# Kernel optimization log

Hardware: AMD Instinct MI355X
Metric: run time of the kernel (lower is better)

Reference implementation:

```python
import jax, jax.numpy as jnp
import numpy as np

B, N, M, D, HEADS, L, DFF, TSTEPS = 8, 1024, 512, 128, 8, 6, 512, 100
S = N + M
HD = D // HEADS


def _layer_norm(x, g, b):
    mu = jnp.mean(x, axis=-1, keepdims=True)
    var = jnp.var(x, axis=-1, keepdims=True)
    return (x - mu) * jax.lax.rsqrt(var + 1e-5) * g + b


def setup_inputs() -> dict:
    rng = np.random.default_rng(0)
    # sparse parity-check matrix, ~6 ones per check row
    H = (rng.random((M, N)) < 6.0 / N).astype(np.float32)
    # create_mask with n_rings=1: eye(S) plus variable<->check Tanner edges
    conn = np.eye(S, dtype=np.float32)
    conn[N:, :N] = np.maximum(conn[N:, :N], H)
    conn[:N, N:] = np.maximum(conn[:N, N:], H.T)
    mask = ~(conn > 0)  # True = attention blocked (src_mask semantics)

    key = jax.random.key(0)
    ks = jax.random.split(key, 16)
    s = 0.05  # weight init scale ~ 1/sqrt(d_model)
    return {
        "r_t": jax.random.normal(ks[0], (B, N), jnp.float32),
        "t": jax.random.randint(ks[1], (B,), 0, TSTEPS),
        "pcm": jnp.asarray(H.astype(np.int32)),
        "mask": jnp.asarray(mask),
        "src_embed": jax.random.uniform(ks[2], (S, D), jnp.float32),
        "time_table": jax.random.normal(ks[3], (TSTEPS, D), jnp.float32),
        "Wq": jax.random.normal(ks[4], (L, D, D), jnp.float32) * s,
        "Wk": jax.random.normal(ks[5], (L, D, D), jnp.float32) * s,
        "Wv": jax.random.normal(ks[6], (L, D, D), jnp.float32) * s,
        "Wo": jax.random.normal(ks[7], (L, D, D), jnp.float32) * s,
        "W1": jax.random.normal(ks[8], (L, D, DFF), jnp.float32) * s,
        "W2": jax.random.normal(ks[9], (L, DFF, D), jnp.float32) * s,
        "g1": jnp.ones((L, D), jnp.float32),
        "b1": jnp.zeros((L, D), jnp.float32),
        "g2": jnp.ones((L, D), jnp.float32),
        "b2": jnp.zeros((L, D), jnp.float32),
        "fc_w": jax.random.normal(ks[10], (D, 1), jnp.float32) * s,
        "fc_b": jnp.zeros((1,), jnp.float32),
    }


def reference(r_t, t, pcm, mask, src_embed, time_table, Wq, Wk, Wv, Wo,
              W1, W2, g1, b1, g2, b2, fc_w, fc_b):
    # to_bin: BPSK sign -> bit {0,1}
    bits = 0.5 * (1.0 - jnp.sign(r_t))                       # [B, N]
    syn = (bits @ pcm.T.astype(jnp.float32)) % 2.0           # mod-2 syndrome [B, M]
    nodes = jnp.concatenate([jnp.abs(r_t), syn], axis=-1)    # [B, S]
    x = src_embed[None, :, :] * nodes[:, :, None]            # [B, S, D]
    te = time_table[t]                                       # [B, D] time embedding
    x = te[:, None, :] * x                                   # time-modulated input
    bias = jnp.where(mask, -1e9, 0.0)[None, None]            # [1, 1, S, S]
    inv_sqrt_hd = 1.0 / jnp.sqrt(jnp.float32(HD))
    for l in range(L):
        h = _layer_norm(x, g1[l], b1[l])
        q = (h @ Wq[l]).reshape(B, S, HEADS, HD)
        k = (h @ Wk[l]).reshape(B, S, HEADS, HD)
        v = (h @ Wv[l]).reshape(B, S, HEADS, HD)
        scores = jnp.einsum('bqhd,bkhd->bhqk', q, k) * inv_sqrt_hd + bias
        p = jax.nn.softmax(scores, axis=-1)
        o = jnp.einsum('bhqk,bkhd->bqhd', p, v).reshape(B, S, D)
        x = x + o @ Wo[l]
        # FiLM-style time conditioning on the FFN branch
        h2 = _layer_norm(x, g2[l], b2[l]) * te[:, None, :]
        x = x + jax.nn.relu(h2 @ W1[l]) @ W2[l]
    return x @ fc_w + fc_b                                   # z_hat [B, S, 1]
```

## Files before the change

### kernel.cpp

```cpp
#include <hip/hip_runtime.h>
#include <cmath>
#include <cstdint>

constexpr int B_ = 8, N_ = 1024, M_ = 512, D_ = 128, S_ = 1536, L_ = 6, DFF_ = 512;
constexpr int ROWS = B_ * S_;
constexpr int MAXDEG = 64;
constexpr int LKEY = 32;
constexpr int RPB  = 48;
constexpr int NBLK = ROWS / RPB;
constexpr int BPB  = S_ / RPB;
constexpr int NTILE = 12;
constexpr int TILE  = 128 * 128;
constexpr int KVSZ  = ROWS * 256;

typedef __bf16 bf16x8 __attribute__((ext_vector_type(8)));
typedef float  f32x4  __attribute__((ext_vector_type(4)));
typedef unsigned short u16x8 __attribute__((ext_vector_type(8)));

__device__ inline unsigned short f2bf(float f) {
  unsigned u = __float_as_uint(f);
  u += 0x7fffu + ((u >> 16) & 1u);
  return (unsigned short)(u >> 16);
}
__device__ inline float bf2f(unsigned short u) {
  return __uint_as_float(((unsigned)u) << 16);
}

__device__ __forceinline__ void async_ld16(const unsigned short* g, unsigned short* l) {
  __builtin_amdgcn_global_load_lds(
      (const __attribute__((address_space(1))) unsigned int*)(uintptr_t)g,
      (__attribute__((address_space(3))) unsigned int*)(unsigned)(uintptr_t)l,
      16, 0, 0);
}
__device__ __forceinline__ void issue_tile(const unsigned short* tp, unsigned short* bs,
                                           int w, int lane) {
  for (int c = w; c < 32; c += 6)
    async_ld16(tp + c * 512 + lane * 8, bs + c * 512);
}

__global__ void adj_init(int* __restrict__ adj, int* __restrict__ adjcnt) {
  int s = blockIdx.x * blockDim.x + threadIdx.x;
  if (s < S_) { adj[s * MAXDEG] = s; adjcnt[s] = 1; }
}
__global__ void adj_build(const int* __restrict__ pcm, int* __restrict__ adj,
                          int* __restrict__ adjcnt) {
  int c = blockIdx.x;
  int lane = threadIdx.x;
  const int* row = pcm + c * N_;
  for (int base = 0; base < N_; base += 64) {
    int k = base + lane;
    if (row[k] != 0) {
      int s1 = atomicAdd(&adjcnt[N_ + c], 1);
      if (s1 < MAXDEG) adj[(N_ + c) * MAXDEG + s1] = k;
      int s2 = atomicAdd(&adjcnt[k], 1);
      if (s2 < MAXDEG) adj[k * MAXDEG + s2] = N_ + c;
    }
  }
}

__global__ void xinit_kernel(const float* __restrict__ r_t, const int* __restrict__ adj,
                             const int* __restrict__ adjcnt, const float* __restrict__ se,
                             const int* __restrict__ tt, const float* __restrict__ table,
                             float* __restrict__ x, unsigned* __restrict__ barrier_cnt) {
  int bs = blockIdx.x;
  int b = bs / S_, s = bs % S_;
  int d = threadIdx.x;
  if (bs < 8 && d == 0)
    __hip_atomic_store(barrier_cnt + bs * 32, 0u, __ATOMIC_RELAXED, __HIP_MEMORY_SCOPE_AGENT);
  float node;
  if (s < N_) {
    node = fabsf(r_t[b * N_ + s]);
  } else {
    int cnt = adjcnt[s]; cnt = cnt < MAXDEG ? cnt : MAXDEG;
    float sum = 0.f;
    for (int j = 0; j < cnt; ++j) {
      int k = adj[s * MAXDEG + j];
      if (k < N_) {
        float r = r_t[b * N_ + k];
        sum += (r < 0.f) ? 1.f : (r > 0.f ? 0.f : 0.5f);
      }
    }
    node = fmodf(sum, 2.0f);
  }
  x[(size_t)bs * D_ + d] = table[tt[b] * D_ + d] * se[s * D_ + d] * node;
}

constexpr int WLAYER = NTILE * TILE;

__global__ void wconv_kernel(const float* __restrict__ Wq, const float* __restrict__ Wk,
                             const float* __restrict__ Wv, const float* __restrict__ Wo,
                             const float* __restrict__ W1, const float* __restrict__ W2,
                             unsigned short* __restrict__ out) {
  __shared__ unsigned short tl[128 * 130];
  int bid = blockIdx.x;
  int l = bid / NTILE, tile = bid % NTILE;
  const float* src;
  int rstride, coff = 0;
  if (tile == 0)      { src = Wk + (size_t)l * D_ * D_;  rstride = D_; }
  else if (tile == 1) { src = Wv + (size_t)l * D_ * D_;  rstride = D_; }
  else if (tile == 2) { src = Wq + (size_t)l * D_ * D_;  rstride = D_; }
  else if (tile == 3) { src = Wo + (size_t)l * D_ * D_;  rstride = D_; }
  else {
    int c = (tile - 4) >> 1;
    if (((tile - 4) & 1) == 0) { src = W1 + (size_t)l * D_ * DFF_; rstride = DFF_; coff = c * 128; }
    else                       { src = W2 + (size_t)l * DFF_ * D_ + (size_t)c * 128 * D_; rstride = D_; }
  }
  for (int i = threadIdx.x; i < 16384; i += 256) {
    int kd = i >> 7, rr = i & 127;
    tl[kd * 130 + rr] = f2bf(src[(size_t)kd * rstride + coff + rr]);
  }
  __syncthreads();
  unsigned short* o = out + (size_t)bid * TILE;
  for (int i = threadIdx.x; i < 16384; i += 256) {
    int rr = i >> 7;
    int sw = (i >> 3) & 15, e = i & 7;
    int kd = (sw ^ (rr & 15)) * 8 + e;
    o[i] = tl[kd * 130 + rr];
  }
}

__device__ __forceinline__ void mfma4(const unsigned short* As, const unsigned short* Bs,
                                      int rowbase, int colbase, int quad, int l16,
                                      f32x4 (&acc)[4]) {
#pragma unroll
  for (int kk = 0; kk < 4; ++kk) {
    int cb = kk * 4 + quad;
    int row = rowbase + l16;
    bf16x8 a = __builtin_bit_cast(bf16x8, *(const uint4*)&As[row * 128 + ((cb ^ (row & 15)) << 3)]);
    bf16x8 bb[4];
#pragma unroll
    for (int ct = 0; ct < 4; ++ct) {
      int n = colbase + ct * 16 + l16;
      bb[ct] = __builtin_bit_cast(bf16x8, *(const uint4*)&Bs[n * 128 + ((cb ^ (n & 15)) << 3)]);
    }
#pragma unroll
    for (int ct = 0; ct < 4; ++ct)
      acc[ct] = __builtin_amdgcn_mfma_f32_16x16x32_bf16(a, bb[ct], acc[ct], 0, 0, 0);
  }
}

__device__ __forceinline__ void grid_barrier(unsigned* cnt, unsigned target) {
  __syncthreads();
  if (threadIdx.x == 0) {
    __hip_atomic_fetch_add(cnt, 1u, __ATOMIC_RELAXED, __HIP_MEMORY_SCOPE_AGENT);
    while (__hip_atomic_load(cnt, __ATOMIC_RELAXED, __HIP_MEMORY_SCOPE_AGENT) < target)
      __builtin_amdgcn_s_sleep(4);
  }
  __syncthreads();
}

__global__ void __launch_bounds__(384) mega_kernel(
    const float* __restrict__ x0, unsigned short* __restrict__ kvbase,
    const unsigned short* __restrict__ wbf,
    const float* __restrict__ g1, const float* __restrict__ b1,
    const float* __restrict__ g2, const float* __restrict__ b2,
    const int* __restrict__ tt, const float* __restrict__ table,
    const int* __restrict__ adj, const int* __restrict__ adjc,
    const float* __restrict__ fcw, const float* __restrict__ fcb,
    float* __restrict__ out, unsigned* barrier_cnt) {
  __shared__ unsigned short As[RPB * 128];
  __shared__ unsigned short Bs[3][TILE];
  __shared__ unsigned short Cs[RPB * 128];
  __shared__ unsigned short KVs[RPB * 256];
  __shared__ float red1[2][RPB], red2[2][RPB];
  __shared__ int sKeys[RPB * LKEY];
  __shared__ int sCnt[RPB];
  const int row0 = blockIdx.x * RPB;
  const int b = row0 / S_;
  const int bS = b * S_;
  const int t = threadIdx.x, w = t >> 6, lane = t & 63, quad = lane >> 4, l16 = lane & 15;
  const int wr = w >> 1, wc = w & 1;
  const int rowbase = wr * 16, colbase = wc * 64;
  const int tbase = tt[b] * D_;
  unsigned* bcnt = barrier_cnt + b * 32;

  issue_tile(wbf + 0 * TILE, Bs[0], w, lane);
  issue_tile(wbf + 1 * TILE, Bs[1], w, lane);
  issue_tile(wbf + 2 * TILE, Bs[2], w, lane);

  f32x4 xreg[4];
#pragma unroll
  for (int ct = 0; ct < 4; ++ct)
#pragma unroll
    for (int i = 0; i < 4; ++i) {
      int row = row0 + rowbase + quad * 4 + i;
      int col = colbase + ct * 16 + l16;
      xreg[ct][i] = x0[(size_t)row * D_ + col];
    }
  if (t < RPB) {
    int c = adjc[row0 + t - bS];
    sCnt[t] = c < MAXDEG ? c : MAXDEG;
  }
  for (int i = t; i < RPB * LKEY; i += 384) {
    int r = i / LKEY, j = i % LKEY;
    sKeys[i] = adj[(row0 + r - bS) * MAXDEG + j];
  }

  for (int l = 0; l < L_; ++l) {
    const unsigned short* wt = wbf + (size_t)l * WLAYER;
    const float* g1l = g1 + l * D_;
    const float* b1l = b1 + l * D_;
    const float* g2l = g2 + l * D_;
    const float* b2l = b2 + l * D_;
    unsigned short* kv = kvbase + (size_t)l * KVSZ;

    float mu1[4], rs1[4];
#pragma unroll
    for (int i = 0; i < 4; ++i) {
      float s = 0.f, sq = 0.f;
#pragma unroll
      for (int ct = 0; ct < 4; ++ct) { s += xreg[ct][i]; sq += xreg[ct][i] * xreg[ct][i]; }
      for (int off = 1; off < 16; off <<= 1) { s += __shfl_xor(s, off); sq += __shfl_xor(sq, off); }
      if (l16 == 0) { red1[wc][rowbase + quad * 4 + i] = s; red2[wc][rowbase + quad * 4 + i] = sq; }
    }
    __syncthreads();
#pragma unroll
    for (int i = 0; i < 4; ++i) {
      int r = rowbase + quad * 4 + i;
      float mu = (red1[0][r] + red1[1][r]) * (1.f / 128.f);
      float var = (red2[0][r] + red2[1][r]) * (1.f / 128.f) - mu * mu;
      mu1[i] = mu;
      rs1[i] = rsqrtf(var + 1e-5f);
    }
#pragma unroll
    for (int ct = 0; ct < 4; ++ct)
#pragma unroll
      for (int i = 0; i < 4; ++i) {
        int rowL = rowbase + quad * 4 + i;
        int col = colbase + ct * 16 + l16;
        float h = (xreg[ct][i] - mu1[i]) * rs1[i] * g1l[col] + b1l[col];
        As[rowL * 128 + (((col >> 3) ^ (rowL & 15)) << 3) + (col & 7)] = f2bf(h);
      }
    __syncthreads();

    {
      f32x4 acc[4];
#pragma unroll
      for (int j = 0; j < 4; ++j) acc[j] = f32x4{0.f, 0.f, 0.f, 0.f};
      mfma4(As, Bs[0], rowbase, colbase, quad, l16, acc);
#pragma unroll
      for (int ct = 0; ct < 4; ++ct)
#pragma unroll
        for (int i = 0; i < 4; ++i) {
          int rowL = rowbase + quad * 4 + i;
          KVs[rowL * 256 + colbase + ct * 16 + l16] = f2bf(acc[ct][i]);
        }
    }
    {
      f32x4 acc[4];
#pragma unroll
      for (int j = 0; j < 4; ++j) acc[j] = f32x4{0.f, 0.f, 0.f, 0.f};
      mfma4(As, Bs[1], rowbase, colbase, quad, l16, acc);
#pragma unroll
      for (int ct = 0; ct < 4; ++ct)
#pragma unroll
        for (int i = 0; i < 4; ++i) {
          int rowL = rowbase + quad * 4 + i;
          KVs[rowL * 256 + 128 + colbase + ct * 16 + l16] = f2bf(acc[ct][i]);
        }
    }
    {
      f32x4 acc[4];
#pragma unroll
      for (int j = 0; j < 4; ++j) acc[j] = f32x4{0.f, 0.f, 0.f, 0.f};
      mfma4(As, Bs[2], rowbase, colbase, quad, l16, acc);
#pragma unroll
      for (int ct = 0; ct < 4; ++ct)
#pragma unroll
        for (int i = 0; i < 4; ++i) {
          int rowL = rowbase + quad * 4 + i;
          int col = colbase + ct * 16 + l16;
          Cs[rowL * 128 + (((col >> 3) ^ (rowL & 15)) << 3) + (col & 7)] = f2bf(acc[ct][i]);
        }
    }
    __syncthreads();
    for (int i = t; i < RPB * 128; i += 384) {
      int rL = i >> 7, cw = i & 127;
      unsigned u = *(const unsigned*)&KVs[rL * 256 + cw * 2];
      __hip_atomic_store((unsigned*)&kv[(size_t)(row0 + rL) * 256 + cw * 2],
                         u, __ATOMIC_RELAXED, __HIP_MEMORY_SCOPE_AGENT);
    }

    grid_barrier(bcnt, (unsigned)(BPB * (l + 1)));

    issue_tile(wt + 3 * TILE, Bs[0], w, lane);
    issue_tile(wt + 4 * TILE, Bs[1], w, lane);
    issue_tile(wt + 5 * TILE, Bs[2], w, lane);

    {
      const int rL = t >> 3, h = t & 7;
      const int s = row0 + rL - bS;
      const int cnt = sCnt[rL];
      float q[16];
      {
        u16x8 qa = *(const u16x8*)&Cs[rL * 128 + (((2 * h) ^ (rL & 15)) << 3)];
        u16x8 qb = *(const u16x8*)&Cs[rL * 128 + (((2 * h + 1) ^ (rL & 15)) << 3)];
#pragma unroll
        for (int j = 0; j < 8; ++j) { q[j] = bf2f(qa[j]); q[8 + j] = bf2f(qb[j]); }
      }
      float m = -1e30f, lsum = 0.f;
      float o16[16];
#pragma unroll
      for (int j = 0; j < 16; ++j) o16[j] = 0.f;
      for (int jb = 0; jb < cnt; jb += 4) {
        u16x8 K[4][2], V[4][2];
#pragma unroll
        for (int u = 0; u < 4; ++u) {
          int j = jb + u;
          int key = 0;
          if (j < cnt) key = (j < LKEY) ? sKeys[rL * LKEY + j] : adj[s * MAXDEG + j];
          const u16x8* kp = (const u16x8*)(kv + (size_t)(bS + key) * 256 + h * 16);
          K[u][0] = kp[0];  K[u][1] = kp[1];
          V[u][0] = kp[16]; V[u][1] = kp[17];
        }
#pragma unroll
        for (int u = 0; u < 4; ++u) {
          float dot = 0.f;
#pragma unroll
          for (int j = 0; j < 8; ++j) {
            dot = fmaf(q[j], bf2f(K[u][0][j]), dot);
            dot = fmaf(q[8 + j], bf2f(K[u][1][j]), dot);
          }
          dot *= 0.25f;
          if (jb + u >= cnt) dot = -1e30f;
          const float mn = fmaxf(m, dot);
          const float rescale = __expf(m - mn);
          const float e = __expf(dot - mn);
          lsum = lsum * rescale + e;
#pragma unroll
          for (int j = 0; j < 8; ++j) {
            o16[j]     = o16[j]     * rescale + e * bf2f(V[u][0][j]);
            o16[8 + j] = o16[8 + j] * rescale + e * bf2f(V[u][1][j]);
          }
          m = mn;
        }
      }
      const float inv = 1.f / lsum;
      u16x8 pk0, pk1;
#pragma unroll
      for (int j = 0; j < 8; ++j) {
        pk0[j] = f2bf(o16[j] * inv);
        pk1[j] = f2bf(o16[8 + j] * inv);
      }
      *(u16x8*)&As[rL * 128 + (((2 * h) ^ (rL & 15)) << 3)] = pk0;
      *(u16x8*)&As[rL * 128 + (((2 * h + 1) ^ (rL & 15)) << 3)] = pk1;
    }
    __syncthreads();

    f32x4 acc1[4];
#pragma unroll
    for (int j = 0; j < 4; ++j) acc1[j] = f32x4{0.f, 0.f, 0.f, 0.f};
    mfma4(As, Bs[0], rowbase, colbase, quad, l16, acc1);
    f32x4 xp[4];
#pragma unroll
    for (int ct = 0; ct < 4; ++ct)
#pragma unroll
      for (int i = 0; i < 4; ++i) xp[ct][i] = xreg[ct][i] + acc1[ct][i];
    float mu_[4], rs_[4];
#pragma unroll
    for (int i = 0; i < 4; ++i) {
      float s = 0.f, sq = 0.f;
#pragma unroll
      for (int ct = 0; ct < 4; ++ct) { s += xp[ct][i]; sq += xp[ct][i] * xp[ct][i]; }
      for (int off = 1; off < 16; off <<= 1) { s += __shfl_xor(s, off); sq += __shfl_xor(sq, off); }
      if (l16 == 0) { red1[wc][rowbase + quad * 4 + i] = s; red2[wc][rowbase + quad * 4 + i] = sq; }
    }
    __syncthreads();
#pragma unroll
    for (int i = 0; i < 4; ++i) {
      int r = rowbase + quad * 4 + i;
      float mu = (red1[0][r] + red1[1][r]) * (1.f / 128.f);
      float var = (red2[0][r] + red2[1][r]) * (1.f / 128.f) - mu * mu;
      mu_[i] = mu;
      rs_[i] = rsqrtf(var + 1e-5f);
    }
#pragma unroll
    for (int ct = 0; ct < 4; ++ct)
#pragma unroll
      for (int i = 0; i < 4; ++i) {
        int rowL = rowbase + quad * 4 + i;
        int col = colbase + ct * 16 + l16;
        float h2 = (xp[ct][i] - mu_[i]) * rs_[i] * g2l[col] + b2l[col];
        h2 *= table[tbase + col];
        As[rowL * 128 + (((col >> 3) ^ (rowL & 15)) << 3) + (col & 7)] = f2bf(h2);
      }
    __syncthreads();

    f32x4 acc2[4];
#pragma unroll
    for (int j = 0; j < 4; ++j) acc2[j] = f32x4{0.f, 0.f, 0.f, 0.f};
    const int bufW1[4] = {1, 0, 2, 1};
    const int bufW2[4] = {2, 1, 0, 2};
#pragma unroll
    for (int c = 0; c < 4; ++c) {
      f32x4 accF[4];
#pragma unroll
      for (int j = 0; j < 4; ++j) accF[j] = f32x4{0.f, 0.f, 0.f, 0.f};
      mfma4(As, Bs[bufW1[c]], rowbase, colbase, quad, l16, accF);
#pragma unroll
      for (int ct = 0; ct < 4; ++ct)
#pragma unroll
        for (int i = 0; i < 4; ++i) {
          int rowL = rowbase + quad * 4 + i;
          int col = colbase + ct * 16 + l16;
          Cs[rowL * 128 + (((col >> 3) ^ (rowL & 15)) << 3) + (col & 7)] =
              f2bf(fmaxf(accF[ct][i], 0.f));
        }
      __syncthreads();
      if (c < 3) issue_tile(wt + (4 + 2 * (c + 1)) * TILE, Bs[bufW1[c + 1]], w, lane);
      else if (l < L_ - 1) issue_tile(wt + WLAYER + 0 * TILE, Bs[0], w, lane);
      mfma4(Cs, Bs[bufW2[c]], rowbase, colbase, quad, l16, acc2);
      __syncthreads();
      if (c < 3) issue_tile(wt + (5 + 2 * (c + 1)) * TILE, Bs[bufW2[c + 1]], w, lane);
      else if (l < L_ - 1) {
        issue_tile(wt + WLAYER + 1 * TILE, Bs[1], w, lane);
        issue_tile(wt + WLAYER + 2 * TILE, Bs[2], w, lane);
      }
    }
    if (l < L_ - 1) {
#pragma unroll
      for (int ct = 0; ct < 4; ++ct)
#pragma unroll
        for (int i = 0; i < 4; ++i) xreg[ct][i] = xp[ct][i] + acc2[ct][i];
    } else {
      float pr[4] = {0.f, 0.f, 0.f, 0.f};
#pragma unroll
      for (int ct = 0; ct < 4; ++ct)
#pragma unroll
        for (int i = 0; i < 4; ++i)
          pr[i] += (xp[ct][i] + acc2[ct][i]) * fcw[colbase + ct * 16 + l16];
#pragma unroll
      for (int i = 0; i < 4; ++i) {
        float s = pr[i];
        for (int off = 1; off < 16; off <<= 1) s += __shfl_xor(s, off);
        if (l16 == 0) red1[wc][rowbase + quad * 4 + i] = s;
      }
      __syncthreads();
      if (wc == 0 && l16 == 0)
#pragma unroll
        for (int i = 0; i < 4; ++i) {
          int r = rowbase + quad * 4 + i;
          out[row0 + r] = red1[0][r] + red1[1][r] + fcb[0];
        }
    }
  }
}

extern "C" void kernel_launch(void* const* d_in, const int* in_sizes, int n_in,
                              void* d_out, int out_size, void* d_ws, size_t ws_size,
                              hipStream_t stream) {
  const float* r_t       = (const float*)d_in[0];
  const int*   t         = (const int*)d_in[1];
  const int*   pcm       = (const int*)d_in[2];
  const float* src_embed = (const float*)d_in[4];
  const float* time_tab  = (const float*)d_in[5];
  const float* Wq = (const float*)d_in[6];
  const float* Wk = (const float*)d_in[7];
  const float* Wv = (const float*)d_in[8];
  const float* Wo = (const float*)d_in[9];
  const float* W1 = (const float*)d_in[10];
  const float* W2 = (const float*)d_in[11];
  const float* g1 = (const float*)d_in[12];
  const float* b1 = (const float*)d_in[13];
  const float* g2 = (const float*)d_in[14];
  const float* b2 = (const float*)d_in[15];
  const float* fc_w = (const float*)d_in[16];
  const float* fc_b = (const float*)d_in[17];
  float* out = (float*)d_out;

  char* ws = (char*)d_ws;
  size_t off = 0;
  auto alloc = [&](size_t bytes) -> void* {
    void* p = ws + off;
    off = (off + bytes + 255) & ~(size_t)255;
    return p;
  };
  float*          x    = (float*)alloc((size_t)ROWS * D_ * 4);
  unsigned short* kv   = (unsigned short*)alloc((size_t)L_ * KVSZ * 2);
  int*            adj  = (int*)alloc((size_t)S_ * MAXDEG * 4);
  int*            adjc = (int*)alloc((size_t)S_ * 4);
  unsigned short* wbf  = (unsigned short*)alloc((size_t)L_ * WLAYER * 2);
  unsigned*       bcnt = (unsigned*)alloc(8 * 32 * 4);

  adj_init<<<(S_ + 255) / 256, 256, 0, stream>>>(adj, adjc);
  adj_build<<<M_, 64, 0, stream>>>(pcm, adj, adjc);
  wconv_kernel<<<L_ * NTILE, 256, 0, stream>>>(Wq, Wk, Wv, Wo, W1, W2, wbf);
  xinit_kernel<<<ROWS, 128, 0, stream>>>(r_t, adj, adjc, src_embed, t, time_tab, x, bcnt);

  mega_kernel<<<NBLK, 384, 0, stream>>>(x, kv, wbf, g1, b1, g2, b2,
                                        t, time_tab, adj, adjc, fc_w, fc_b, out, bcnt);
}
```

Baseline: 260.0 us.

## Fuse adjacency init into weight conversion and input embedding into mega kernel

Removes the adj_init and xinit kernels. Adjacency initialisation and the barrier-counter reset move into the first blocks of wconv_kernel. The syndrome and embedding computation of the initial x moves into mega_kernel's prologue using the staged adjacency keys. This cuts two kernel launches and the write and re-read of the full fp32 x buffer. In exchange, each mega_kernel block does a short serial per-row syndrome loop before its first layer.

Measured after the change: 255.3 us. About the same (-1.8%).

```diff
diff --git a/kernel.cpp b/kernel.cpp
--- a/kernel.cpp
+++ b/kernel.cpp
@@ -38,10 +38,6 @@
     async_ld16(tp + c * 512 + lane * 8, bs + c * 512);
 }
 
-__global__ void adj_init(int* __restrict__ adj, int* __restrict__ adjcnt) {
-  int s = blockIdx.x * blockDim.x + threadIdx.x;
-  if (s < S_) { adj[s * MAXDEG] = s; adjcnt[s] = 1; }
-}
 __global__ void adj_build(const int* __restrict__ pcm, int* __restrict__ adj,
                           int* __restrict__ adjcnt) {
   int c = blockIdx.x;
@@ -58,41 +54,22 @@
   }
 }
 
-__global__ void xinit_kernel(const float* __restrict__ r_t, const int* __restrict__ adj,
-                             const int* __restrict__ adjcnt, const float* __restrict__ se,
-                             const int* __restrict__ tt, const float* __restrict__ table,
-                             float* __restrict__ x, unsigned* __restrict__ barrier_cnt) {
-  int bs = blockIdx.x;
-  int b = bs / S_, s = bs % S_;
-  int d = threadIdx.x;
-  if (bs < 8 && d == 0)
-    __hip_atomic_store(barrier_cnt + bs * 32, 0u, __ATOMIC_RELAXED, __HIP_MEMORY_SCOPE_AGENT);
-  float node;
-  if (s < N_) {
-    node = fabsf(r_t[b * N_ + s]);
-  } else {
-    int cnt = adjcnt[s]; cnt = cnt < MAXDEG ? cnt : MAXDEG;
-    float sum = 0.f;
-    for (int j = 0; j < cnt; ++j) {
-      int k = adj[s * MAXDEG + j];
-      if (k < N_) {
-        float r = r_t[b * N_ + k];
-        sum += (r < 0.f) ? 1.f : (r > 0.f ? 0.f : 0.5f);
-      }
-    }
-    node = fmodf(sum, 2.0f);
-  }
-  x[(size_t)bs * D_ + d] = table[tt[b] * D_ + d] * se[s * D_ + d] * node;
-}
-
 constexpr int WLAYER = NTILE * TILE;
 
 __global__ void wconv_kernel(const float* __restrict__ Wq, const float* __restrict__ Wk,
                              const float* __restrict__ Wv, const float* __restrict__ Wo,
                              const float* __restrict__ W1, const float* __restrict__ W2,
-                             unsigned short* __restrict__ out) {
+                             unsigned short* __restrict__ out, int* __restrict__ adj,
+                             int* __restrict__ adjcnt, unsigned* __restrict__ barrier_cnt) {
   __shared__ unsigned short tl[128 * 130];
   int bid = blockIdx.x;
+  if (bid < 6) {
+    int s = bid * 256 + threadIdx.x;
+    if (s < S_) { adj[s * MAXDEG] = s; adjcnt[s] = 1; }
+  }
+  if (bid == 6 && threadIdx.x < 8)
+    __hip_atomic_store(barrier_cnt + threadIdx.x * 32, 0u,
+                       __ATOMIC_RELAXED, __HIP_MEMORY_SCOPE_AGENT);
   int l = bid / NTILE, tile = bid % NTILE;
   const float* src;
   int rstride, coff = 0;
@@ -150,8 +127,8 @@
 }
 
 __global__ void __launch_bounds__(384) mega_kernel(
-    const float* __restrict__ x0, unsigned short* __restrict__ kvbase,
-    const unsigned short* __restrict__ wbf,
+    const float* __restrict__ r_t, const float* __restrict__ se,
+    unsigned short* __restrict__ kvbase, const unsigned short* __restrict__ wbf,
     const float* __restrict__ g1, const float* __restrict__ b1,
     const float* __restrict__ g2, const float* __restrict__ b2,
     const int* __restrict__ tt, const float* __restrict__ table,
@@ -163,6 +140,7 @@
   __shared__ unsigned short Cs[RPB * 128];
   __shared__ unsigned short KVs[RPB * 256];
   __shared__ float red1[2][RPB], red2[2][RPB];
+  __shared__ float nodeS[RPB];
   __shared__ int sKeys[RPB * LKEY];
   __shared__ int sCnt[RPB];
   const int row0 = blockIdx.x * RPB;
@@ -178,15 +156,6 @@
   issue_tile(wbf + 1 * TILE, Bs[1], w, lane);
   issue_tile(wbf + 2 * TILE, Bs[2], w, lane);
 
-  f32x4 xreg[4];
-#pragma unroll
-  for (int ct = 0; ct < 4; ++ct)
-#pragma unroll
-    for (int i = 0; i < 4; ++i) {
-      int row = row0 + rowbase + quad * 4 + i;
-      int col = colbase + ct * 16 + l16;
-      xreg[ct][i] = x0[(size_t)row * D_ + col];
-    }
   if (t < RPB) {
     int c = adjc[row0 + t - bS];
     sCnt[t] = c < MAXDEG ? c : MAXDEG;
@@ -195,6 +164,37 @@
     int r = i / LKEY, j = i % LKEY;
     sKeys[i] = adj[(row0 + r - bS) * MAXDEG + j];
   }
+  __syncthreads();
+  if (t < RPB) {
+    int s = row0 + t - bS;
+    float node;
+    if (s < N_) {
+      node = fabsf(r_t[b * N_ + s]);
+    } else {
+      int cnt = sCnt[t];
+      float sum = 0.f;
+      for (int j = 0; j < cnt; ++j) {
+        int k = (j < LKEY) ? sKeys[t * LKEY + j] : adj[s * MAXDEG + j];
+        if (k < N_) {
+          float r = r_t[b * N_ + k];
+          sum += (r < 0.f) ? 1.f : (r > 0.f ? 0.f : 0.5f);
+        }
+      }
+      node = fmodf(sum, 2.0f);
+    }
+    nodeS[t] = node;
+  }
+  __syncthreads();
+  f32x4 xreg[4];
+#pragma unroll
+  for (int ct = 0; ct < 4; ++ct)
+#pragma unroll
+    for (int i = 0; i < 4; ++i) {
+      int rowL = rowbase + quad * 4 + i;
+      int s = row0 + rowL - bS;
+      int col = colbase + ct * 16 + l16;
+      xreg[ct][i] = table[tbase + col] * se[(size_t)s * D_ + col] * nodeS[rowL];
+    }
 
   for (int l = 0; l < L_; ++l) {
     const unsigned short* wt = wbf + (size_t)l * WLAYER;
@@ -475,18 +475,14 @@
     off = (off + bytes + 255) & ~(size_t)255;
     return p;
   };
-  float*          x    = (float*)alloc((size_t)ROWS * D_ * 4);
   unsigned short* kv   = (unsigned short*)alloc((size_t)L_ * KVSZ * 2);
   int*            adj  = (int*)alloc((size_t)S_ * MAXDEG * 4);
   int*            adjc = (int*)alloc((size_t)S_ * 4);
   unsigned short* wbf  = (unsigned short*)alloc((size_t)L_ * WLAYER * 2);
   unsigned*       bcnt = (unsigned*)alloc(8 * 32 * 4);
 
-  adj_init<<<(S_ + 255) / 256, 256, 0, stream>>>(adj, adjc);
+  wconv_kernel<<<L_ * NTILE, 256, 0, stream>>>(Wq, Wk, Wv, Wo, W1, W2, wbf, adj, adjc, bcnt);
   adj_build<<<M_, 64, 0, stream>>>(pcm, adj, adjc);
-  wconv_kernel<<<L_ * NTILE, 256, 0, stream>>>(Wq, Wk, Wv, Wo, W1, W2, wbf);
-  xinit_kernel<<<ROWS, 128, 0, stream>>>(r_t, adj, adjc, src_embed, t, time_tab, x, bcnt);
-
-  mega_kernel<<<NBLK, 384, 0, stream>>>(x, kv, wbf, g1, b1, g2, b2,
+  mega_kernel<<<NBLK, 384, 0, stream>>>(r_t, src_embed, kv, wbf, g1, b1, g2, b2,
                                         t, time_tab, adj, adjc, fc_w, fc_b, out, bcnt);
 }
```
